# Optimization experiments

Measured on AMD Instinct MI355X. Metric: run time of the kernel, lower is better.

Reference implementation:

```python
import jax, jax.numpy as jnp
import numpy as np

CHUNK_SIZE = 64
EPS = 1e-6


def setup_inputs() -> dict:
    key = jax.random.key(0)
    ks = jax.random.split(key, 5)
    B, NH, S, DH = 2, 16, 4096, 64
    return {
        "q": jax.random.normal(ks[0], (B, NH, S, DH), dtype=jnp.float32),
        "k": jax.random.normal(ks[1], (B, NH, S, DH), dtype=jnp.float32),
        "v": jax.random.normal(ks[2], (B, NH, S, DH), dtype=jnp.float32),
        "igate_preact": jax.random.normal(ks[3], (B, NH, S), dtype=jnp.float32),
        "fgate_preact": jax.random.normal(ks[4], (B, NH, S), dtype=jnp.float32),
    }


def _mlstm_intra(q, k, v, ig, fg, chunk_size, eps):
    # q,k,v: [B,NH,S,DH]; ig,fg: [B,NH,S]
    B, NH, S, DH = q.shape
    L = chunk_size
    NC = S // L
    qc = q.reshape(B, NH, NC, L, DH)
    kc = k.reshape(B, NH, NC, L, DH)
    vc = v.reshape(B, NH, NC, L, DH)
    igc = ig.reshape(B, NH, NC, L)
    fgc = fg.reshape(B, NH, NC, L)

    # log forget gates and their within-chunk cumulative sums
    log_fg = jax.nn.log_sigmoid(fgc)                      # [B,NH,NC,L]
    log_fg_cum = jnp.cumsum(log_fg, axis=-1)              # [B,NH,NC,L]

    # gated decay matrix: logD[i,j] = sum_{t=j+1..i} log f_t + i_j  for j<=i
    log_fg_mat = log_fg_cum[..., :, None] - log_fg_cum[..., None, :]  # [B,NH,NC,L,L]
    log_D = log_fg_mat + igc[..., None, :]
    causal = jnp.tril(jnp.ones((L, L), dtype=bool))
    log_D = jnp.where(causal, log_D, -jnp.inf)

    # stabilizer (row-wise max)
    m = jnp.max(log_D, axis=-1)                           # [B,NH,NC,L]
    D = jnp.exp(log_D - m[..., None])                     # [B,NH,NC,L,L]

    # QK scores scaled, gated by decay matrix
    scale = 1.0 / jnp.sqrt(jnp.asarray(DH, dtype=q.dtype))
    scores = jnp.einsum("bncld,bncsd->bncls", qc, kc) * scale
    C = scores * D                                        # [B,NH,NC,L,L]

    # stabilized normalizer: max(|row sum|, exp(-m))
    n = jnp.maximum(jnp.abs(jnp.sum(C, axis=-1)), jnp.exp(-m))  # [B,NH,NC,L]
    h = jnp.einsum("bncls,bncsd->bncld", C, vc) / (n[..., None] + eps)
    return h.reshape(B, NH, S, DH)


def reference(q, k, v, igate_preact, fgate_preact):
    return _mlstm_intra(q, k, v, igate_preact, fgate_preact, CHUNK_SIZE, EPS)
```

## Files before the change

### kernel.cpp

```cpp
#include <hip/hip_runtime.h>
#include <hip/hip_bf16.h>
#include <math.h>
#include <stdint.h>

namespace {

typedef __bf16 bf16x8 __attribute__((ext_vector_type(8)));
typedef float f32x4 __attribute__((ext_vector_type(4)));

constexpr int L = 64;
constexpr int DH = 64;

__device__ __forceinline__ int kkey(int r) { return (r ^ (r >> 2)) & 7; }
__device__ __forceinline__ int swzC(int r, int col) {
  return r * 128 + ((((col >> 3) ^ kkey(r)) & 7) << 4) + (col & 7) * 2;
}

__device__ __forceinline__ unsigned short bfbits(float f) {
  __bf16 h = (__bf16)f;
  return __builtin_bit_cast(unsigned short, h);
}
__device__ __forceinline__ __bf16 tobf(float f) { return (__bf16)f; }
__device__ __forceinline__ unsigned long long pack4(float a, float b, float c,
                                                    float d) {
  return (unsigned long long)bfbits(a) | ((unsigned long long)bfbits(b) << 16) |
         ((unsigned long long)bfbits(c) << 32) |
         ((unsigned long long)bfbits(d) << 48);
}

__device__ __forceinline__ void gload16(const float* gsrc, float* ldst) {
  __builtin_amdgcn_global_load_lds(
      (const __attribute__((address_space(1))) uint32_t*)gsrc,
      (__attribute__((address_space(3))) uint32_t*)ldst, 16, 0, 0);
}

__global__ __launch_bounds__(256, 4) void mlstm_mfma(
    const float* __restrict__ q, const float* __restrict__ k,
    const float* __restrict__ v, const float* __restrict__ ig,
    const float* __restrict__ fg, float* __restrict__ out) {

  __shared__ __align__(16) float k_lds[64 * 64];
  __shared__ __align__(16) float v_lds[64 * 64];
  __shared__ __align__(16) char cs_raw[4][16 * 128];

  const int tid = threadIdx.x;
  const int w = tid >> 6;
  const int lane = tid & 63;
  const int m = lane & 15;
  const int g = lane >> 4;
  const size_t cbase = (size_t)blockIdx.x * (L * DH);
  const size_t gb = (size_t)blockIdx.x * L;

  const float fgv = fg[gb + lane];
  const float igv = ig[gb + lane];

  {
    const int rsub = lane >> 4;
    const int slot = lane & 15;
#pragma unroll
    for (int s = 0; s < 4; ++s) {
      const int it = w * 4 + s;
      const int r = it * 4 + rsub;
      const int coff = r * 64 + ((slot ^ kkey(r)) << 2);
      gload16(k + cbase + coff, &k_lds[it * 256]);
      gload16(v + cbase + coff, &v_lds[it * 256]);
    }
  }

  float4 qbuf[2][2];
#pragma unroll
  for (int kb = 0; kb < 2; ++kb) {
    const int off = (w * 16 + m) * 64 + kb * 32 + g * 8;
    qbuf[kb][0] = *(const float4*)(q + cbase + off);
    qbuf[kb][1] = *(const float4*)(q + cbase + off + 4);
  }

  float ea, eb, em;
  {
    const float lf = fminf(fgv, 0.f) - log1pf(__expf(-fabsf(fgv)));
    float cum = lf;
#pragma unroll
    for (int o = 1; o < 64; o <<= 1) {
      const float t = __shfl_up(cum, o, 64);
      if (lane >= o) cum += t;
    }
    const float a = igv - cum;
    float b = a;
#pragma unroll
    for (int o = 1; o < 64; o <<= 1) {
      const float t = __shfl_up(b, o, 64);
      if (lane >= o) b = fmaxf(b, t);
    }
    const float bmax = __shfl(b, 63, 64);
    ea = 0.125f * __expf(a - bmax);
    eb = __expf(bmax - b);
    em = __expf(-(b + cum));
  }

  bf16x8 qf[2];
#pragma unroll
  for (int kb = 0; kb < 2; ++kb) {
    const float4 q0 = qbuf[kb][0], q1 = qbuf[kb][1];
    qf[kb] = bf16x8{tobf(q0.x), tobf(q0.y), tobf(q0.z), tobf(q0.w),
                    tobf(q1.x), tobf(q1.y), tobf(q1.z), tobf(q1.w)};
  }

  asm volatile("s_waitcnt vmcnt(0)" ::: "memory");
  __syncthreads();

  bf16x8 kf[4][2];
#pragma unroll
  for (int rb = 0; rb < 4; ++rb) {
    if (rb <= w) {
#pragma unroll
      for (int kb = 0; kb < 2; ++kb) {
        const int row = rb * 16 + m;
        const int c4 = kb * 8 + g * 2;
        const int o0 = row * 64 + (((c4 + 0) ^ kkey(row)) << 2);
        const int o1 = row * 64 + (((c4 + 1) ^ kkey(row)) << 2);
        const f32x4 ka = *(const f32x4*)&k_lds[o0];
        const f32x4 kb4 = *(const f32x4*)&k_lds[o1];
        kf[rb][kb] =
            bf16x8{tobf(ka[0]), tobf(ka[1]), tobf(ka[2]), tobf(ka[3]),
                   tobf(kb4[0]), tobf(kb4[1]), tobf(kb4[2]), tobf(kb4[3])};
      }
    }
  }

  const int njb = (w >= 2) ? 2 : 1;
  bf16x8 vfr[4][2];
#pragma unroll
  for (int db = 0; db < 4; ++db) {
    const int d = db * 16 + m;
    const int dslot = d >> 2;
    const int dsub = d & 3;
#pragma unroll
    for (int jb = 0; jb < 2; ++jb) {
      if (jb < njb) {
        float tv[8];
#pragma unroll
        for (int t = 0; t < 8; ++t) {
          const int j = jb * 32 + g * 8 + t;
          tv[t] = v_lds[j * 64 + ((dslot ^ kkey(j)) << 2) + dsub];
        }
        vfr[db][jb] =
            bf16x8{tobf(tv[0]), tobf(tv[1]), tobf(tv[2]), tobf(tv[3]),
                   tobf(tv[4]), tobf(tv[5]), tobf(tv[6]), tobf(tv[7])};
      }
    }
  }

  f32x4 st[4];
#pragma unroll
  for (int rb = 0; rb < 4; ++rb) {
    if (rb <= w) {
      f32x4 acc = {0.f, 0.f, 0.f, 0.f};
      acc = __builtin_amdgcn_mfma_f32_16x16x32_bf16(kf[rb][0], qf[0], acc, 0, 0, 0);
      acc = __builtin_amdgcn_mfma_f32_16x16x32_bf16(kf[rb][1], qf[1], acc, 0, 0, 0);
      st[rb] = acc;
    }
  }

  char* cw = cs_raw[w];
  const int i = w * 16 + m;
  const float ebv = __shfl(eb, i, 64);
  const float emv = __shfl(em, i, 64);
  float ea_j[4][4];
#pragma unroll
  for (int rb = 0; rb < 4; ++rb)
#pragma unroll
    for (int e = 0; e < 4; ++e)
      ea_j[rb][e] = __shfl(ea, rb * 16 + g * 4 + e, 64);

  float rs = 0.f;
  const int rbfill = w | 1;
#pragma unroll
  for (int rb = 0; rb < 4; ++rb) {
    if (rb > rbfill) continue;
    unsigned long long wp = 0ull;
    if (rb <= w) {
      float vv[4];
#pragma unroll
      for (int e = 0; e < 4; ++e) {
        const int j = rb * 16 + g * 4 + e;
        vv[e] = (j <= i) ? st[rb][e] * ea_j[rb][e] * ebv : 0.f;
        rs += vv[e];
      }
      wp = pack4(vv[0], vv[1], vv[2], vv[3]);
    }
    *(unsigned long long*)(cw + swzC(m, rb * 16 + g * 4)) = wp;
  }
  rs += __shfl_xor(rs, 16, 64);
  rs += __shfl_xor(rs, 32, 64);
  const float invv = 1.f / (fmaxf(fabsf(rs), emv) + 1e-6f);

  const bf16x8 c0 = *(const bf16x8*)(cw + swzC(m, g * 8));
  f32x4 acc[4];
#pragma unroll
  for (int db = 0; db < 4; ++db) {
    f32x4 z = {0.f, 0.f, 0.f, 0.f};
    acc[db] = __builtin_amdgcn_mfma_f32_16x16x32_bf16(vfr[db][0], c0, z, 0, 0, 0);
  }
  if (w >= 2) {
    const bf16x8 c1 = *(const bf16x8*)(cw + swzC(m, 32 + g * 8));
#pragma unroll
    for (int db = 0; db < 4; ++db)
      acc[db] = __builtin_amdgcn_mfma_f32_16x16x32_bf16(vfr[db][1], c1, acc[db], 0, 0, 0);
  }

  float* op = out + cbase + i * 64 + g * 4;
#pragma unroll
  for (int db = 0; db < 4; ++db) {
    const f32x4 hv = acc[db];
    *(float4*)(op + db * 16) =
        make_float4(hv[0] * invv, hv[1] * invv, hv[2] * invv, hv[3] * invv);
  }
}

}

extern "C" void kernel_launch(void* const* d_in, const int* in_sizes, int n_in,
                              void* d_out, int out_size, void* d_ws,
                              size_t ws_size, hipStream_t stream) {
  const float* q = (const float*)d_in[0];
  const float* k = (const float*)d_in[1];
  const float* v = (const float*)d_in[2];
  const float* ig = (const float*)d_in[3];
  const float* fg = (const float*)d_in[4];
  float* out = (float*)d_out;

  const int total = in_sizes[0];
  const int nchunks = total / (L * DH);
  mlstm_mfma<<<dim3(nchunks), dim3(256), 0, stream>>>(q, k, v, ig, fg, out);
}
```

Measured before the change: 27.91 us.

## Process four chunks per block with double-buffered K/V prefetch

Each block now loops over four consecutive chunks instead of one. While the current chunk is being computed, the next chunk's K/V tiles are loaded into a second LDS buffer and its Q, ig and fg values into registers, so global memory latency overlaps with MFMA work. The cost is twice the LDS per block and the launch-bounds occupancy hint drops from 4 to 2. That leaves fewer resident waves to hide latency, and the grid shrinks by a factor of four.

```diff
diff --git a/kernel.cpp b/kernel.cpp
--- a/kernel.cpp
+++ b/kernel.cpp
@@ -8,8 +8,7 @@
 typedef __bf16 bf16x8 __attribute__((ext_vector_type(8)));
 typedef float f32x4 __attribute__((ext_vector_type(4)));
 
-constexpr int L = 64;
-constexpr int DH = 64;
+constexpr int NLOC = 4;
 
 __device__ __forceinline__ int kkey(int r) { return (r ^ (r >> 2)) & 7; }
 __device__ __forceinline__ int swzC(int r, int col) {
@@ -34,13 +33,13 @@
       (__attribute__((address_space(3))) uint32_t*)ldst, 16, 0, 0);
 }
 
-__global__ __launch_bounds__(256, 4) void mlstm_mfma(
+__global__ __launch_bounds__(256, 2) void mlstm_pipe(
     const float* __restrict__ q, const float* __restrict__ k,
     const float* __restrict__ v, const float* __restrict__ ig,
     const float* __restrict__ fg, float* __restrict__ out) {
 
-  __shared__ __align__(16) float k_lds[64 * 64];
-  __shared__ __align__(16) float v_lds[64 * 64];
+  __shared__ __align__(16) float k_lds[2][64 * 64];
+  __shared__ __align__(16) float v_lds[2][64 * 64];
   __shared__ __align__(16) char cs_raw[4][16 * 128];
 
   const int tid = threadIdx.x;
@@ -48,173 +47,186 @@
   const int lane = tid & 63;
   const int m = lane & 15;
   const int g = lane >> 4;
-  const size_t cbase = (size_t)blockIdx.x * (L * DH);
-  const size_t gb = (size_t)blockIdx.x * L;
-
-  const float fgv = fg[gb + lane];
-  const float igv = ig[gb + lane];
-
-  {
-    const int rsub = lane >> 4;
-    const int slot = lane & 15;
-#pragma unroll
-    for (int s = 0; s < 4; ++s) {
-      const int it = w * 4 + s;
-      const int r = it * 4 + rsub;
-      const int coff = r * 64 + ((slot ^ kkey(r)) << 2);
-      gload16(k + cbase + coff, &k_lds[it * 256]);
-      gload16(v + cbase + coff, &v_lds[it * 256]);
+  const int rsub = lane >> 4;
+  const int slot = lane & 15;
+  const size_t chunk0 = (size_t)blockIdx.x * NLOC;
+
+  float fgv[2], igv[2];
+  float4 qb[2][2][2];
+
+#define STAGE(buf, cn)                                                    \
+  do {                                                                    \
+    const size_t cb_ = (size_t)(cn)*4096;                                 \
+    fgv[buf] = fg[(size_t)(cn)*64 + lane];                                \
+    igv[buf] = ig[(size_t)(cn)*64 + lane];                                \
+    _Pragma("unroll") for (int s = 0; s < 4; ++s) {                       \
+      const int it = w * 4 + s;                                           \
+      const int r = it * 4 + rsub;                                        \
+      const int coff = r * 64 + ((slot ^ kkey(r)) << 2);                  \
+      gload16(k + cb_ + coff, &k_lds[buf][it * 256]);                     \
+      gload16(v + cb_ + coff, &v_lds[buf][it * 256]);                     \
+    }                                                                     \
+    _Pragma("unroll") for (int kb = 0; kb < 2; ++kb) {                    \
+      const int off = (w * 16 + m) * 64 + kb * 32 + g * 8;                \
+      qb[buf][kb][0] = *(const float4*)(q + cb_ + off);                   \
+      qb[buf][kb][1] = *(const float4*)(q + cb_ + off + 4);               \
+    }                                                                     \
+  } while (0)
+
+  STAGE(0, chunk0);
+
+#pragma unroll
+  for (int n = 0; n < NLOC; ++n) {
+    const int cur = n & 1;
+    const int nxt = cur ^ 1;
+
+    asm volatile("s_waitcnt vmcnt(0)" ::: "memory");
+    __syncthreads();
+
+    if (n + 1 < NLOC) {
+      if (nxt) STAGE(1, chunk0 + n + 1); else STAGE(0, chunk0 + n + 1);
+    }
+
+    float ea, eb, em;
+    {
+      const float fv = fgv[cur];
+      const float lf = fminf(fv, 0.f) - log1pf(__expf(-fabsf(fv)));
+      float cum = lf;
+#pragma unroll
+      for (int o = 1; o < 64; o <<= 1) {
+        const float t = __shfl_up(cum, o, 64);
+        if (lane >= o) cum += t;
+      }
+      const float a = igv[cur] - cum;
+      float b = a;
+#pragma unroll
+      for (int o = 1; o < 64; o <<= 1) {
+        const float t = __shfl_up(b, o, 64);
+        if (lane >= o) b = fmaxf(b, t);
+      }
+      const float bmax = __shfl(b, 63, 64);
+      ea = 0.125f * __expf(a - bmax);
+      eb = __expf(bmax - b);
+      em = __expf(-(b + cum));
+    }
+
+    bf16x8 qf[2];
+#pragma unroll
+    for (int kb = 0; kb < 2; ++kb) {
+      const float4 q0 = qb[cur][kb][0], q1 = qb[cur][kb][1];
+      qf[kb] = bf16x8{tobf(q0.x), tobf(q0.y), tobf(q0.z), tobf(q0.w),
+                      tobf(q1.x), tobf(q1.y), tobf(q1.z), tobf(q1.w)};
+    }
+
+    bf16x8 kf[4][2];
+#pragma unroll
+    for (int rb = 0; rb < 4; ++rb) {
+      if (rb <= w) {
+#pragma unroll
+        for (int kb = 0; kb < 2; ++kb) {
+          const int row = rb * 16 + m;
+          const int c4 = kb * 8 + g * 2;
+          const int o0 = row * 64 + (((c4 + 0) ^ kkey(row)) << 2);
+          const int o1 = row * 64 + (((c4 + 1) ^ kkey(row)) << 2);
+          const f32x4 ka = *(const f32x4*)&k_lds[cur][o0];
+          const f32x4 kb4 = *(const f32x4*)&k_lds[cur][o1];
+          kf[rb][kb] =
+              bf16x8{tobf(ka[0]), tobf(ka[1]), tobf(ka[2]), tobf(ka[3]),
+                     tobf(kb4[0]), tobf(kb4[1]), tobf(kb4[2]), tobf(kb4[3])};
+        }
+      }
+    }
+
+    const int njb = (w >= 2) ? 2 : 1;
+    bf16x8 vfr[4][2];
+#pragma unroll
+    for (int db = 0; db < 4; ++db) {
+      const int d = db * 16 + m;
+      const int dslot = d >> 2;
+      const int dsub = d & 3;
+#pragma unroll
+      for (int jb = 0; jb < 2; ++jb) {
+        if (jb < njb) {
+          float tv[8];
+#pragma unroll
+          for (int t = 0; t < 8; ++t) {
+            const int j = jb * 32 + g * 8 + t;
+            tv[t] = v_lds[cur][j * 64 + ((dslot ^ kkey(j)) << 2) + dsub];
+          }
+          vfr[db][jb] =
+              bf16x8{tobf(tv[0]), tobf(tv[1]), tobf(tv[2]), tobf(tv[3]),
+                     tobf(tv[4]), tobf(tv[5]), tobf(tv[6]), tobf(tv[7])};
+        }
+      }
+    }
+
+    f32x4 st[4];
+#pragma unroll
+    for (int rb = 0; rb < 4; ++rb) {
+      if (rb <= w) {
+        f32x4 acc = {0.f, 0.f, 0.f, 0.f};
+        acc = __builtin_amdgcn_mfma_f32_16x16x32_bf16(kf[rb][0], qf[0], acc, 0, 0, 0);
+        acc = __builtin_amdgcn_mfma_f32_16x16x32_bf16(kf[rb][1], qf[1], acc, 0, 0, 0);
+        st[rb] = acc;
+      }
+    }
+
+    char* cw = cs_raw[w];
+    const int i = w * 16 + m;
+    const float ebv = __shfl(eb, i, 64);
+    const float emv = __shfl(em, i, 64);
+    float ea_j[4][4];
+#pragma unroll
+    for (int rb = 0; rb < 4; ++rb)
+#pragma unroll
+      for (int e = 0; e < 4; ++e)
+        ea_j[rb][e] = __shfl(ea, rb * 16 + g * 4 + e, 64);
+
+    float rs = 0.f;
+    const int rbfill = w | 1;
+#pragma unroll
+    for (int rb = 0; rb < 4; ++rb) {
+      if (rb > rbfill) continue;
+      unsigned long long wp = 0ull;
+      if (rb <= w) {
+        float vv[4];
+#pragma unroll
+        for (int e = 0; e < 4; ++e) {
+          const int j = rb * 16 + g * 4 + e;
+          vv[e] = (j <= i) ? st[rb][e] * ea_j[rb][e] * ebv : 0.f;
+          rs += vv[e];
+        }
+        wp = pack4(vv[0], vv[1], vv[2], vv[3]);
+      }
+      *(unsigned long long*)(cw + swzC(m, rb * 16 + g * 4)) = wp;
+    }
+    rs += __shfl_xor(rs, 16, 64);
+    rs += __shfl_xor(rs, 32, 64);
+    const float invv = 1.f / (fmaxf(fabsf(rs), emv) + 1e-6f);
+
+    const bf16x8 c0 = *(const bf16x8*)(cw + swzC(m, g * 8));
+    f32x4 acc[4];
+#pragma unroll
+    for (int db = 0; db < 4; ++db) {
+      f32x4 z = {0.f, 0.f, 0.f, 0.f};
+      acc[db] = __builtin_amdgcn_mfma_f32_16x16x32_bf16(vfr[db][0], c0, z, 0, 0, 0);
+    }
+    if (w >= 2) {
+      const bf16x8 c1 = *(const bf16x8*)(cw + swzC(m, 32 + g * 8));
+#pragma unroll
+      for (int db = 0; db < 4; ++db)
+        acc[db] = __builtin_amdgcn_mfma_f32_16x16x32_bf16(vfr[db][1], c1, acc[db], 0, 0, 0);
+    }
+
+    float* op = out + (chunk0 + n) * 4096 + i * 64 + g * 4;
+#pragma unroll
+    for (int db = 0; db < 4; ++db) {
+      const f32x4 hv = acc[db];
+      *(float4*)(op + db * 16) =
+          make_float4(hv[0] * invv, hv[1] * invv, hv[2] * invv, hv[3] * invv);
     }
   }
-
-  float4 qbuf[2][2];
-#pragma unroll
-  for (int kb = 0; kb < 2; ++kb) {
-    const int off = (w * 16 + m) * 64 + kb * 32 + g * 8;
-    qbuf[kb][0] = *(const float4*)(q + cbase + off);
-    qbuf[kb][1] = *(const float4*)(q + cbase + off + 4);
-  }
-
-  float ea, eb, em;
-  {
-    const float lf = fminf(fgv, 0.f) - log1pf(__expf(-fabsf(fgv)));
-    float cum = lf;
-#pragma unroll
-    for (int o = 1; o < 64; o <<= 1) {
-      const float t = __shfl_up(cum, o, 64);
-      if (lane >= o) cum += t;
-    }
-    const float a = igv - cum;
-    float b = a;
-#pragma unroll
-    for (int o = 1; o < 64; o <<= 1) {
-      const float t = __shfl_up(b, o, 64);
-      if (lane >= o) b = fmaxf(b, t);
-    }
-    const float bmax = __shfl(b, 63, 64);
-    ea = 0.125f * __expf(a - bmax);
-    eb = __expf(bmax - b);
-    em = __expf(-(b + cum));
-  }
-
-  bf16x8 qf[2];
-#pragma unroll
-  for (int kb = 0; kb < 2; ++kb) {
-    const float4 q0 = qbuf[kb][0], q1 = qbuf[kb][1];
-    qf[kb] = bf16x8{tobf(q0.x), tobf(q0.y), tobf(q0.z), tobf(q0.w),
-                    tobf(q1.x), tobf(q1.y), tobf(q1.z), tobf(q1.w)};
-  }
-
-  asm volatile("s_waitcnt vmcnt(0)" ::: "memory");
-  __syncthreads();
-
-  bf16x8 kf[4][2];
-#pragma unroll
-  for (int rb = 0; rb < 4; ++rb) {
-    if (rb <= w) {
-#pragma unroll
-      for (int kb = 0; kb < 2; ++kb) {
-        const int row = rb * 16 + m;
-        const int c4 = kb * 8 + g * 2;
-        const int o0 = row * 64 + (((c4 + 0) ^ kkey(row)) << 2);
-        const int o1 = row * 64 + (((c4 + 1) ^ kkey(row)) << 2);
-        const f32x4 ka = *(const f32x4*)&k_lds[o0];
-        const f32x4 kb4 = *(const f32x4*)&k_lds[o1];
-        kf[rb][kb] =
-            bf16x8{tobf(ka[0]), tobf(ka[1]), tobf(ka[2]), tobf(ka[3]),
-                   tobf(kb4[0]), tobf(kb4[1]), tobf(kb4[2]), tobf(kb4[3])};
-      }
-    }
-  }
-
-  const int njb = (w >= 2) ? 2 : 1;
-  bf16x8 vfr[4][2];
-#pragma unroll
-  for (int db = 0; db < 4; ++db) {
-    const int d = db * 16 + m;
-    const int dslot = d >> 2;
-    const int dsub = d & 3;
-#pragma unroll
-    for (int jb = 0; jb < 2; ++jb) {
-      if (jb < njb) {
-        float tv[8];
-#pragma unroll
-        for (int t = 0; t < 8; ++t) {
-          const int j = jb * 32 + g * 8 + t;
-          tv[t] = v_lds[j * 64 + ((dslot ^ kkey(j)) << 2) + dsub];
-        }
-        vfr[db][jb] =
-            bf16x8{tobf(tv[0]), tobf(tv[1]), tobf(tv[2]), tobf(tv[3]),
-                   tobf(tv[4]), tobf(tv[5]), tobf(tv[6]), tobf(tv[7])};
-      }
-    }
-  }
-
-  f32x4 st[4];
-#pragma unroll
-  for (int rb = 0; rb < 4; ++rb) {
-    if (rb <= w) {
-      f32x4 acc = {0.f, 0.f, 0.f, 0.f};
-      acc = __builtin_amdgcn_mfma_f32_16x16x32_bf16(kf[rb][0], qf[0], acc, 0, 0, 0);
-      acc = __builtin_amdgcn_mfma_f32_16x16x32_bf16(kf[rb][1], qf[1], acc, 0, 0, 0);
-      st[rb] = acc;
-    }
-  }
-
-  char* cw = cs_raw[w];
-  const int i = w * 16 + m;
-  const float ebv = __shfl(eb, i, 64);
-  const float emv = __shfl(em, i, 64);
-  float ea_j[4][4];
-#pragma unroll
-  for (int rb = 0; rb < 4; ++rb)
-#pragma unroll
-    for (int e = 0; e < 4; ++e)
-      ea_j[rb][e] = __shfl(ea, rb * 16 + g * 4 + e, 64);
-
-  float rs = 0.f;
-  const int rbfill = w | 1;
-#pragma unroll
-  for (int rb = 0; rb < 4; ++rb) {
-    if (rb > rbfill) continue;
-    unsigned long long wp = 0ull;
-    if (rb <= w) {
-      float vv[4];
-#pragma unroll
-      for (int e = 0; e < 4; ++e) {
-        const int j = rb * 16 + g * 4 + e;
-        vv[e] = (j <= i) ? st[rb][e] * ea_j[rb][e] * ebv : 0.f;
-        rs += vv[e];
-      }
-      wp = pack4(vv[0], vv[1], vv[2], vv[3]);
-    }
-    *(unsigned long long*)(cw + swzC(m, rb * 16 + g * 4)) = wp;
-  }
-  rs += __shfl_xor(rs, 16, 64);
-  rs += __shfl_xor(rs, 32, 64);
-  const float invv = 1.f / (fmaxf(fabsf(rs), emv) + 1e-6f);
-
-  const bf16x8 c0 = *(const bf16x8*)(cw + swzC(m, g * 8));
-  f32x4 acc[4];
-#pragma unroll
-  for (int db = 0; db < 4; ++db) {
-    f32x4 z = {0.f, 0.f, 0.f, 0.f};
-    acc[db] = __builtin_amdgcn_mfma_f32_16x16x32_bf16(vfr[db][0], c0, z, 0, 0, 0);
-  }
-  if (w >= 2) {
-    const bf16x8 c1 = *(const bf16x8*)(cw + swzC(m, 32 + g * 8));
-#pragma unroll
-    for (int db = 0; db < 4; ++db)
-      acc[db] = __builtin_amdgcn_mfma_f32_16x16x32_bf16(vfr[db][1], c1, acc[db], 0, 0, 0);
-  }
-
-  float* op = out + cbase + i * 64 + g * 4;
-#pragma unroll
-  for (int db = 0; db < 4; ++db) {
-    const f32x4 hv = acc[db];
-    *(float4*)(op + db * 16) =
-        make_float4(hv[0] * invv, hv[1] * invv, hv[2] * invv, hv[3] * invv);
-  }
+#undef STAGE
 }
 
 }
@@ -230,6 +242,7 @@
   float* out = (float*)d_out;
 
   const int total = in_sizes[0];
-  const int nchunks = total / (L * DH);
-  mlstm_mfma<<<dim3(nchunks), dim3(256), 0, stream>>>(q, k, v, ig, fg, out);
-}
+  const int nchunks = total / 4096;
+  const int nblocks = nchunks / NLOC;
+  mlstm_pipe<<<dim3(nblocks), dim3(256), 0, stream>>>(q, k, v, ig, fg, out);
+}
```

New measurement: 29.06 us. +4.1%, slower.
